# Kernel optimization log

Hardware: AMD Instinct MI355X
Metric: run time of the kernel (lower is better)

Reference implementation:

```python
import jax, jax.numpy as jnp
import numpy as np


def setup_inputs() -> dict:
    key = jax.random.key(0)
    ks = jax.random.split(key, 6)
    B, d, S = 256, 512, 196  # batch, hidden dim, spatial locations (14x14)
    return {
        "memory_state": jax.random.normal(ks[0], (B, d), dtype=jnp.float32),
        "ctrl_state": jax.random.normal(ks[1], (B, d), dtype=jnp.float32),
        "kb_proj": jax.random.normal(ks[2], (B, d, S), dtype=jnp.float32),
        "W_concat": jax.random.normal(ks[3], (d, d), dtype=jnp.float32) * (1.0 / np.sqrt(d)),
        "b_concat": jax.random.normal(ks[4], (d,), dtype=jnp.float32) * 0.01,
        "w_attn": jax.random.normal(ks[5], (d,), dtype=jnp.float32) * (1.0 / np.sqrt(d)),
    }


def reference(memory_state, ctrl_state, kb_proj, W_concat, b_concat, w_attn):
    # I_elements: [B, S, d] -- elementwise gating of knowledge base by memory
    I_t = memory_state[:, :, None] * kb_proj           # [B, d, S]
    I_t = jnp.transpose(I_t, (0, 2, 1))                # [B, S, d]
    # concat_layer (torch Linear: x @ W^T + b) + residual with kb_proj
    concat = jnp.einsum('bsd,ed->bse', I_t, W_concat) + b_concat
    concat = concat + jnp.transpose(kb_proj, (0, 2, 1))  # [B, S, d]
    # attention logits: (concat * ctrl) @ w_attn -> [B, S]
    rai = jnp.einsum('bsd,d->bs', concat * ctrl_state[:, None, :], w_attn)
    rvi = jax.nn.softmax(rai, axis=1)                  # [B, S]
    # attention-weighted sum over spatial locations -> [B, d]
    read_vector = jnp.einsum('bs,bds->bd', rvi, kb_proj)
    return read_vector
```

## Files before the change

### kernel.cpp

```cpp
#include <hip/hip_runtime.h>
#include <math.h>

#define B 256
#define D 512
#define S 196
#define SQ 49
#define NCH 8

__global__ __launch_bounds__(256, 8) void k_fused_logits(
    const float* __restrict__ kb, const float* __restrict__ mem,
    const float* __restrict__ ctrl, const float* __restrict__ w_attn,
    const float* __restrict__ W, float* __restrict__ rai_part) {
    __shared__ float u_s[D];
    __shared__ float gred[16][64];
    __shared__ float p_s[64];
    __shared__ float part[4][S];
    const int bid = blockIdx.x;
    const int b = bid >> 3, c = bid & 7;
    const int t = threadIdx.x;
    const int w = t >> 6, l = t & 63;

    u_s[t]       = ctrl[(size_t)b * D + t]       * w_attn[t];
    u_s[t + 256] = ctrl[(size_t)b * D + t + 256] * w_attn[t + 256];
    __syncthreads();

    {
        const int q = t & 15, eg = t >> 4;
        float4 g4 = {0.f, 0.f, 0.f, 0.f};
        const float* wbase = W + (size_t)c * 64 + 4 * q;
#pragma unroll 4
        for (int k = 0; k < 32; ++k) {
            const int e = k * 16 + eg;
            const float4 w4 = *(const float4*)(wbase + (size_t)e * D);
            const float uv = u_s[e];
            g4.x += uv * w4.x; g4.y += uv * w4.y;
            g4.z += uv * w4.z; g4.w += uv * w4.w;
        }
        *(float4*)&gred[eg][4 * q] = g4;
    }
    __syncthreads();
    if (t < 64) {
        float g = 0.f;
#pragma unroll
        for (int eg = 0; eg < 16; ++eg) g += gred[eg][t];
        const int d = c * 64 + t;
        p_s[t] = mem[(size_t)b * D + d] * g + u_s[d];
    }
    __syncthreads();

    const float* base = kb + (size_t)b * D * S + (size_t)c * 64 * S;
    if (l < SQ) {
        float4 acc0 = {0.f, 0.f, 0.f, 0.f}, acc1 = {0.f, 0.f, 0.f, 0.f};
        for (int i = 0; i < 8; ++i) {
            const int r0 = w * 16 + i, r1 = w * 16 + 8 + i;
            const float4 v0 = *(const float4*)(base + (size_t)r0 * S + 4 * l);
            const float4 v1 = *(const float4*)(base + (size_t)r1 * S + 4 * l);
            const float pv0 = p_s[r0], pv1 = p_s[r1];
            acc0.x += pv0 * v0.x; acc0.y += pv0 * v0.y;
            acc0.z += pv0 * v0.z; acc0.w += pv0 * v0.w;
            acc1.x += pv1 * v1.x; acc1.y += pv1 * v1.y;
            acc1.z += pv1 * v1.z; acc1.w += pv1 * v1.w;
        }
        part[w][4 * l + 0] = acc0.x + acc1.x;
        part[w][4 * l + 1] = acc0.y + acc1.y;
        part[w][4 * l + 2] = acc0.z + acc1.z;
        part[w][4 * l + 3] = acc0.w + acc1.w;
    }
    __syncthreads();
    if (t < S)
        rai_part[(size_t)bid * S + t] =
            (part[0][t] + part[1][t]) + (part[2][t] + part[3][t]);
}

__global__ __launch_bounds__(256, 8) void k_wsum(
    const float* __restrict__ kb, const float* __restrict__ rai_part,
    float* __restrict__ out) {
    __shared__ float rvi_s[S];
    __shared__ float redm[4], reds[4];
    __shared__ float plds[64 * SQ];
    __shared__ float red2[4][64];
    const int bid = blockIdx.x;
    const int b = bid >> 3, c = bid & 7;
    const int t = threadIdx.x;
    const int w = t >> 6, l = t & 63;

    float rai = -INFINITY;
    if (t < S) {
        float v = 0.f;
#pragma unroll
        for (int k = 0; k < NCH; ++k)
            v += rai_part[((size_t)b * NCH + k) * S + t];
        rai = v;
    }
    float m = rai;
#pragma unroll
    for (int o = 1; o < 64; o <<= 1) m = fmaxf(m, __shfl_xor(m, o, 64));
    if (l == 0) redm[w] = m;
    __syncthreads();
    m = fmaxf(fmaxf(redm[0], redm[1]), fmaxf(redm[2], redm[3]));
    float ex = (t < S) ? __expf(rai - m) : 0.f;
    float sm = ex;
#pragma unroll
    for (int o = 1; o < 64; o <<= 1) sm += __shfl_xor(sm, o, 64);
    if (l == 0) reds[w] = sm;
    __syncthreads();
    const float li = (reds[0] + reds[1]) + (reds[2] + reds[3]);
    if (t < S) rvi_s[t] = ex / li;
    __syncthreads();

    float4 rv = {0.f, 0.f, 0.f, 0.f};
    if (l < SQ) rv = *(const float4*)&rvi_s[4 * l];
    const float* base = kb + (size_t)b * D * S + (size_t)c * 64 * S;
    if (l < SQ) {
#pragma unroll 2
        for (int i = 0; i < 8; ++i) {
            const int r0 = w * 16 + i, r1 = w * 16 + 8 + i;
            const float4 v0 = *(const float4*)(base + (size_t)r0 * S + 4 * l);
            const float4 v1 = *(const float4*)(base + (size_t)r1 * S + 4 * l);
            plds[r0 * SQ + l] =
                rv.x * v0.x + rv.y * v0.y + rv.z * v0.z + rv.w * v0.w;
            plds[r1 * SQ + l] =
                rv.x * v1.x + rv.y * v1.y + rv.z * v1.z + rv.w * v1.w;
        }
    }
    __syncthreads();
    {
        const int row = t & 63, seg = t >> 6;
        const int j0 = (seg * SQ) >> 2, j1 = ((seg + 1) * SQ) >> 2;
        float a = 0.f;
        for (int j = j0; j < j1; ++j) a += plds[row * SQ + j];
        red2[seg][row] = a;
    }
    __syncthreads();
    if (t < 64)
        out[(size_t)b * D + c * 64 + t] =
            (red2[0][t] + red2[1][t]) + (red2[2][t] + red2[3][t]);
}

extern "C" void kernel_launch(void* const* d_in, const int* in_sizes, int n_in,
                              void* d_out, int out_size, void* d_ws, size_t ws_size,
                              hipStream_t stream) {
    const float* mem  = (const float*)d_in[0];
    const float* ctrl = (const float*)d_in[1];
    const float* kb   = (const float*)d_in[2];
    const float* W    = (const float*)d_in[3];
    const float* wat  = (const float*)d_in[5];
    float* out = (float*)d_out;

    float* rai_part = (float*)d_ws;

    k_fused_logits<<<B * NCH, 256, 0, stream>>>(kb, mem, ctrl, wat, W, rai_part);
    k_wsum        <<<B * NCH, 256, 0, stream>>>(kb, rai_part, out);
}
```

Before: 192.0 us.

## Split W-projection into separate batched kernel reusing W across eight batches

```diff
diff --git a/kernel.cpp b/kernel.cpp
--- a/kernel.cpp
+++ b/kernel.cpp
@@ -7,47 +7,48 @@
 #define SQ 49
 #define NCH 8
 
-__global__ __launch_bounds__(256, 8) void k_fused_logits(
-    const float* __restrict__ kb, const float* __restrict__ mem,
-    const float* __restrict__ ctrl, const float* __restrict__ w_attn,
-    const float* __restrict__ W, float* __restrict__ rai_part) {
-    __shared__ float u_s[D];
-    __shared__ float gred[16][64];
+__global__ __launch_bounds__(256) void k_pvec(
+    const float* __restrict__ mem, const float* __restrict__ ctrl,
+    const float* __restrict__ w_attn, const float* __restrict__ W,
+    float* __restrict__ p) {
+    __shared__ float u_s[8][D];
+    const int c = blockIdx.x & 7;
+    const int b0 = (blockIdx.x >> 3) * 8;
+    const int t = threadIdx.x;
+#pragma unroll
+    for (int idx = t; idx < 8 * D; idx += 256) {
+        const int j = idx >> 9, e = idx & (D - 1);
+        u_s[j][e] = ctrl[(size_t)(b0 + j) * D + e] * w_attn[e];
+    }
+    __syncthreads();
+    const int d = t & 63;
+    const int j0 = (t >> 6) * 2, j1 = j0 + 1;
+    const float* wcol = W + (size_t)c * 64 + d;
+    float a0 = 0.f, a1 = 0.f;
+#pragma unroll 4
+    for (int e = 0; e < D; ++e) {
+        const float wv = wcol[(size_t)e * D];
+        a0 += u_s[j0][e] * wv;
+        a1 += u_s[j1][e] * wv;
+    }
+    const int dg = c * 64 + d;
+    p[(size_t)(b0 + j0) * D + dg] =
+        mem[(size_t)(b0 + j0) * D + dg] * a0 + u_s[j0][dg];
+    p[(size_t)(b0 + j1) * D + dg] =
+        mem[(size_t)(b0 + j1) * D + dg] * a1 + u_s[j1][dg];
+}
+
+__global__ __launch_bounds__(256, 8) void k_logits(
+    const float* __restrict__ kb, const float* __restrict__ p,
+    float* __restrict__ rai_part) {
     __shared__ float p_s[64];
     __shared__ float part[4][S];
     const int bid = blockIdx.x;
     const int b = bid >> 3, c = bid & 7;
     const int t = threadIdx.x;
     const int w = t >> 6, l = t & 63;
-
-    u_s[t]       = ctrl[(size_t)b * D + t]       * w_attn[t];
-    u_s[t + 256] = ctrl[(size_t)b * D + t + 256] * w_attn[t + 256];
+    if (t < 64) p_s[t] = p[(size_t)b * D + c * 64 + t];
     __syncthreads();
-
-    {
-        const int q = t & 15, eg = t >> 4;
-        float4 g4 = {0.f, 0.f, 0.f, 0.f};
-        const float* wbase = W + (size_t)c * 64 + 4 * q;
-#pragma unroll 4
-        for (int k = 0; k < 32; ++k) {
-            const int e = k * 16 + eg;
-            const float4 w4 = *(const float4*)(wbase + (size_t)e * D);
-            const float uv = u_s[e];
-            g4.x += uv * w4.x; g4.y += uv * w4.y;
-            g4.z += uv * w4.z; g4.w += uv * w4.w;
-        }
-        *(float4*)&gred[eg][4 * q] = g4;
-    }
-    __syncthreads();
-    if (t < 64) {
-        float g = 0.f;
-#pragma unroll
-        for (int eg = 0; eg < 16; ++eg) g += gred[eg][t];
-        const int d = c * 64 + t;
-        p_s[t] = mem[(size_t)b * D + d] * g + u_s[d];
-    }
-    __syncthreads();
-
     const float* base = kb + (size_t)b * D * S + (size_t)c * 64 * S;
     if (l < SQ) {
         float4 acc0 = {0.f, 0.f, 0.f, 0.f}, acc1 = {0.f, 0.f, 0.f, 0.f};
@@ -147,8 +148,10 @@
     const float* wat  = (const float*)d_in[5];
     float* out = (float*)d_out;
 
-    float* rai_part = (float*)d_ws;
+    float* p        = (float*)d_ws;
+    float* rai_part = p + (size_t)B * D;
 
-    k_fused_logits<<<B * NCH, 256, 0, stream>>>(kb, mem, ctrl, wat, W, rai_part);
-    k_wsum        <<<B * NCH, 256, 0, stream>>>(kb, rai_part, out);
+    k_pvec  <<<256,     256, 0, stream>>>(mem, ctrl, wat, W, p);
+    k_logits<<<B * NCH, 256, 0, stream>>>(kb, p, rai_part);
+    k_wsum  <<<B * NCH, 256, 0, stream>>>(kb, rai_part, out);
 }
```

Result: slower. 244.7 us (+27.5%).

## Split u·W GEMM into batched kernel and fuse logits, softmax, weighted sum per batch

Applied to the files above, without the earlier changes.

```diff
diff --git a/kernel.cpp b/kernel.cpp
--- a/kernel.cpp
+++ b/kernel.cpp
@@ -7,52 +7,73 @@
 #define SQ 49
 #define NCH 8
 
-__global__ __launch_bounds__(256, 8) void k_fused_logits(
-    const float* __restrict__ kb, const float* __restrict__ mem,
+__global__ __launch_bounds__(256) void k_gemm2(
     const float* __restrict__ ctrl, const float* __restrict__ w_attn,
-    const float* __restrict__ W, float* __restrict__ rai_part) {
-    __shared__ float u_s[D];
-    __shared__ float gred[16][64];
-    __shared__ float p_s[64];
-    __shared__ float part[4][S];
-    const int bid = blockIdx.x;
-    const int b = bid >> 3, c = bid & 7;
+    const float* __restrict__ W, float* __restrict__ gpart) {
+    __shared__ float u_s[64][8];
+    const int ce = blockIdx.x >> 6;
+    const int dh = (blockIdx.x >> 5) & 1;
+    const int b0 = (blockIdx.x & 31) * 8;
+    const int t = threadIdx.x;
+    const int d = dh * 256 + t;
+#pragma unroll
+    for (int k = t; k < 512; k += 256) {
+        const int j = k & 7, el = k >> 3;
+        const int e = ce * 64 + el;
+        u_s[el][j] = ctrl[(size_t)(b0 + j) * D + e] * w_attn[e];
+    }
+    __syncthreads();
+    float a[8];
+#pragma unroll
+    for (int j = 0; j < 8; ++j) a[j] = 0.f;
+    for (int e0 = 0; e0 < 64; e0 += 4) {
+        float wv[4];
+#pragma unroll
+        for (int i = 0; i < 4; ++i)
+            wv[i] = W[(size_t)(ce * 64 + e0 + i) * D + d];
+#pragma unroll
+        for (int i = 0; i < 4; ++i) {
+            const float4 ua = *(const float4*)&u_s[e0 + i][0];
+            const float4 ub = *(const float4*)&u_s[e0 + i][4];
+            a[0] += ua.x * wv[i]; a[1] += ua.y * wv[i];
+            a[2] += ua.z * wv[i]; a[3] += ua.w * wv[i];
+            a[4] += ub.x * wv[i]; a[5] += ub.y * wv[i];
+            a[6] += ub.z * wv[i]; a[7] += ub.w * wv[i];
+        }
+    }
+#pragma unroll
+    for (int j = 0; j < 8; ++j)
+        gpart[((size_t)(b0 + j) * NCH + ce) * D + d] = a[j];
+}
+
+struct SmP2 { float plds[256 * SQ]; float red2[4][256]; };
+__global__ __launch_bounds__(1024, 1) void k_batch(
+    const float* __restrict__ kb, const float* __restrict__ gpart,
+    const float* __restrict__ mem, const float* __restrict__ ctrl,
+    const float* __restrict__ w_attn, float* __restrict__ out) {
+    __shared__ float p_s[D];
+    __shared__ float rvi_s[S];
+    __shared__ float redm[4], reds[4];
+    __shared__ union { float part[16][S]; SmP2 p2; } smu;
+    const int b = blockIdx.x;
     const int t = threadIdx.x;
     const int w = t >> 6, l = t & 63;
+    const float* base = kb + (size_t)b * D * S;
 
-    u_s[t]       = ctrl[(size_t)b * D + t]       * w_attn[t];
-    u_s[t + 256] = ctrl[(size_t)b * D + t + 256] * w_attn[t + 256];
-    __syncthreads();
-
-    {
-        const int q = t & 15, eg = t >> 4;
-        float4 g4 = {0.f, 0.f, 0.f, 0.f};
-        const float* wbase = W + (size_t)c * 64 + 4 * q;
-#pragma unroll 4
-        for (int k = 0; k < 32; ++k) {
-            const int e = k * 16 + eg;
-            const float4 w4 = *(const float4*)(wbase + (size_t)e * D);
-            const float uv = u_s[e];
-            g4.x += uv * w4.x; g4.y += uv * w4.y;
-            g4.z += uv * w4.z; g4.w += uv * w4.w;
-        }
-        *(float4*)&gred[eg][4 * q] = g4;
-    }
-    __syncthreads();
-    if (t < 64) {
-        float g = 0.f;
+    if (t < D) {
+        float s = 0.f;
 #pragma unroll
-        for (int eg = 0; eg < 16; ++eg) g += gred[eg][t];
-        const int d = c * 64 + t;
-        p_s[t] = mem[(size_t)b * D + d] * g + u_s[d];
+        for (int ce = 0; ce < NCH; ++ce)
+            s += gpart[((size_t)b * NCH + ce) * D + t];
+        p_s[t] = mem[(size_t)b * D + t] * s +
+                 ctrl[(size_t)b * D + t] * w_attn[t];
     }
     __syncthreads();
 
-    const float* base = kb + (size_t)b * D * S + (size_t)c * 64 * S;
     if (l < SQ) {
         float4 acc0 = {0.f, 0.f, 0.f, 0.f}, acc1 = {0.f, 0.f, 0.f, 0.f};
-        for (int i = 0; i < 8; ++i) {
-            const int r0 = w * 16 + i, r1 = w * 16 + 8 + i;
+        for (int i = 0; i < 16; ++i) {
+            const int r0 = w * 32 + i, r1 = w * 32 + 16 + i;
             const float4 v0 = *(const float4*)(base + (size_t)r0 * S + 4 * l);
             const float4 v1 = *(const float4*)(base + (size_t)r1 * S + 4 * l);
             const float pv0 = p_s[r0], pv1 = p_s[r1];
@@ -61,80 +82,75 @@
             acc1.x += pv1 * v1.x; acc1.y += pv1 * v1.y;
             acc1.z += pv1 * v1.z; acc1.w += pv1 * v1.w;
         }
-        part[w][4 * l + 0] = acc0.x + acc1.x;
-        part[w][4 * l + 1] = acc0.y + acc1.y;
-        part[w][4 * l + 2] = acc0.z + acc1.z;
-        part[w][4 * l + 3] = acc0.w + acc1.w;
+        smu.part[w][4 * l + 0] = acc0.x + acc1.x;
+        smu.part[w][4 * l + 1] = acc0.y + acc1.y;
+        smu.part[w][4 * l + 2] = acc0.z + acc1.z;
+        smu.part[w][4 * l + 3] = acc0.w + acc1.w;
     }
     __syncthreads();
-    if (t < S)
-        rai_part[(size_t)bid * S + t] =
-            (part[0][t] + part[1][t]) + (part[2][t] + part[3][t]);
-}
 
-__global__ __launch_bounds__(256, 8) void k_wsum(
-    const float* __restrict__ kb, const float* __restrict__ rai_part,
-    float* __restrict__ out) {
-    __shared__ float rvi_s[S];
-    __shared__ float redm[4], reds[4];
-    __shared__ float plds[64 * SQ];
-    __shared__ float red2[4][64];
-    const int bid = blockIdx.x;
-    const int b = bid >> 3, c = bid & 7;
-    const int t = threadIdx.x;
-    const int w = t >> 6, l = t & 63;
-
-    float rai = -INFINITY;
+    float rai = -INFINITY, ex = 0.f;
     if (t < S) {
         float v = 0.f;
 #pragma unroll
-        for (int k = 0; k < NCH; ++k)
-            v += rai_part[((size_t)b * NCH + k) * S + t];
+        for (int ww = 0; ww < 16; ++ww) v += smu.part[ww][t];
         rai = v;
     }
-    float m = rai;
+    if (t < 256) {
+        float m = rai;
 #pragma unroll
-    for (int o = 1; o < 64; o <<= 1) m = fmaxf(m, __shfl_xor(m, o, 64));
-    if (l == 0) redm[w] = m;
+        for (int o = 1; o < 64; o <<= 1) m = fmaxf(m, __shfl_xor(m, o, 64));
+        if (l == 0) redm[w] = m;
+    }
     __syncthreads();
-    m = fmaxf(fmaxf(redm[0], redm[1]), fmaxf(redm[2], redm[3]));
-    float ex = (t < S) ? __expf(rai - m) : 0.f;
-    float sm = ex;
+    if (t < 256) {
+        const float m = fmaxf(fmaxf(redm[0], redm[1]), fmaxf(redm[2], redm[3]));
+        ex = (t < S) ? __expf(rai - m) : 0.f;
+        float sm = ex;
 #pragma unroll
-    for (int o = 1; o < 64; o <<= 1) sm += __shfl_xor(sm, o, 64);
-    if (l == 0) reds[w] = sm;
+        for (int o = 1; o < 64; o <<= 1) sm += __shfl_xor(sm, o, 64);
+        if (l == 0) reds[w] = sm;
+    }
     __syncthreads();
-    const float li = (reds[0] + reds[1]) + (reds[2] + reds[3]);
-    if (t < S) rvi_s[t] = ex / li;
+    if (t < S) {
+        const float li = (reds[0] + reds[1]) + (reds[2] + reds[3]);
+        rvi_s[t] = ex / li;
+    }
     __syncthreads();
 
     float4 rv = {0.f, 0.f, 0.f, 0.f};
     if (l < SQ) rv = *(const float4*)&rvi_s[4 * l];
-    const float* base = kb + (size_t)b * D * S + (size_t)c * 64 * S;
-    if (l < SQ) {
+    for (int half = 0; half < 2; ++half) {
+        const int rb = half * 256;
+        if (l < SQ) {
 #pragma unroll 2
-        for (int i = 0; i < 8; ++i) {
-            const int r0 = w * 16 + i, r1 = w * 16 + 8 + i;
-            const float4 v0 = *(const float4*)(base + (size_t)r0 * S + 4 * l);
-            const float4 v1 = *(const float4*)(base + (size_t)r1 * S + 4 * l);
-            plds[r0 * SQ + l] =
-                rv.x * v0.x + rv.y * v0.y + rv.z * v0.z + rv.w * v0.w;
-            plds[r1 * SQ + l] =
-                rv.x * v1.x + rv.y * v1.y + rv.z * v1.z + rv.w * v1.w;
+            for (int i = 0; i < 8; ++i) {
+                const int q0 = w * 16 + i, q1 = w * 16 + 8 + i;
+                const float4 v0 =
+                    *(const float4*)(base + (size_t)(rb + q0) * S + 4 * l);
+                const float4 v1 =
+                    *(const float4*)(base + (size_t)(rb + q1) * S + 4 * l);
+                smu.p2.plds[q0 * SQ + l] =
+                    rv.x * v0.x + rv.y * v0.y + rv.z * v0.z + rv.w * v0.w;
+                smu.p2.plds[q1 * SQ + l] =
+                    rv.x * v1.x + rv.y * v1.y + rv.z * v1.z + rv.w * v1.w;
+            }
         }
+        __syncthreads();
+        {
+            const int r = t & 255, seg = t >> 8;
+            const int j0 = (seg * SQ) >> 2, j1 = ((seg + 1) * SQ) >> 2;
+            float a = 0.f;
+            for (int j = j0; j < j1; ++j) a += smu.p2.plds[r * SQ + j];
+            smu.p2.red2[seg][r] = a;
+        }
+        __syncthreads();
+        if (t < 256)
+            out[(size_t)b * D + rb + t] =
+                (smu.p2.red2[0][t] + smu.p2.red2[1][t]) +
+                (smu.p2.red2[2][t] + smu.p2.red2[3][t]);
+        __syncthreads();
     }
-    __syncthreads();
-    {
-        const int row = t & 63, seg = t >> 6;
-        const int j0 = (seg * SQ) >> 2, j1 = ((seg + 1) * SQ) >> 2;
-        float a = 0.f;
-        for (int j = j0; j < j1; ++j) a += plds[row * SQ + j];
-        red2[seg][row] = a;
-    }
-    __syncthreads();
-    if (t < 64)
-        out[(size_t)b * D + c * 64 + t] =
-            (red2[0][t] + red2[1][t]) + (red2[2][t] + red2[3][t]);
 }
 
 extern "C" void kernel_launch(void* const* d_in, const int* in_sizes, int n_in,
@@ -147,8 +163,8 @@
     const float* wat  = (const float*)d_in[5];
     float* out = (float*)d_out;
 
-    float* rai_part = (float*)d_ws;
+    float* gpart = (float*)d_ws;
 
-    k_fused_logits<<<B * NCH, 256, 0, stream>>>(kb, mem, ctrl, wat, W, rai_part);
-    k_wsum        <<<B * NCH, 256, 0, stream>>>(kb, rai_part, out);
+    k_gemm2<<<512, 256,  0, stream>>>(ctrl, wat, W, gpart);
+    k_batch<<<B,   1024, 0, stream>>>(kb, gpart, mem, ctrl, wat, out);
 }
```

Result: faster. 182.5 us (-4.9%).

## Split W·u matvec into batched GEMM kernel and prefetch kb rows early

Applied to the files above, without the earlier changes.

```diff
diff --git a/kernel.cpp b/kernel.cpp
--- a/kernel.cpp
+++ b/kernel.cpp
@@ -7,64 +7,108 @@
 #define SQ 49
 #define NCH 8
 
-__global__ __launch_bounds__(256, 8) void k_fused_logits(
-    const float* __restrict__ kb, const float* __restrict__ mem,
+__global__ __launch_bounds__(256) void k_gemm2(
     const float* __restrict__ ctrl, const float* __restrict__ w_attn,
-    const float* __restrict__ W, float* __restrict__ rai_part) {
-    __shared__ float u_s[D];
-    __shared__ float gred[16][64];
+    const float* __restrict__ W, float* __restrict__ gpart) {
+    __shared__ float u_s[64][8];
+    const int ce = blockIdx.x >> 6;
+    const int dh = (blockIdx.x >> 5) & 1;
+    const int b0 = (blockIdx.x & 31) * 8;
+    const int t = threadIdx.x;
+    const int d = dh * 256 + t;
+#pragma unroll
+    for (int k = t; k < 512; k += 256) {
+        const int j = k & 7, el = k >> 3;
+        const int e = ce * 64 + el;
+        u_s[el][j] = ctrl[(size_t)(b0 + j) * D + e] * w_attn[e];
+    }
+    __syncthreads();
+    float a[8];
+#pragma unroll
+    for (int j = 0; j < 8; ++j) a[j] = 0.f;
+    for (int e0 = 0; e0 < 64; e0 += 4) {
+        float wv[4];
+#pragma unroll
+        for (int i = 0; i < 4; ++i)
+            wv[i] = W[(size_t)(ce * 64 + e0 + i) * D + d];
+#pragma unroll
+        for (int i = 0; i < 4; ++i) {
+            const float4 ua = *(const float4*)&u_s[e0 + i][0];
+            const float4 ub = *(const float4*)&u_s[e0 + i][4];
+            a[0] += ua.x * wv[i]; a[1] += ua.y * wv[i];
+            a[2] += ua.z * wv[i]; a[3] += ua.w * wv[i];
+            a[4] += ub.x * wv[i]; a[5] += ub.y * wv[i];
+            a[6] += ub.z * wv[i]; a[7] += ub.w * wv[i];
+        }
+    }
+#pragma unroll
+    for (int j = 0; j < 8; ++j)
+        gpart[((size_t)(b0 + j) * NCH + ce) * D + d] = a[j];
+}
+
+__global__ __launch_bounds__(256, 4) void k_logits(
+    const float* __restrict__ kb, const float* __restrict__ gpart,
+    const float* __restrict__ mem, const float* __restrict__ ctrl,
+    const float* __restrict__ w_attn, float* __restrict__ rai_part) {
+    __shared__ float ph[4][64];
     __shared__ float p_s[64];
     __shared__ float part[4][S];
     const int bid = blockIdx.x;
     const int b = bid >> 3, c = bid & 7;
     const int t = threadIdx.x;
     const int w = t >> 6, l = t & 63;
-
-    u_s[t]       = ctrl[(size_t)b * D + t]       * w_attn[t];
-    u_s[t + 256] = ctrl[(size_t)b * D + t + 256] * w_attn[t + 256];
-    __syncthreads();
-
+    const float* base = kb + (size_t)b * D * S + (size_t)c * 64 * S;
+    const int r0 = w * 16;
+
+    float4 h0, h1, h2, h3;
+    if (l < SQ) {
+        h0 = *(const float4*)(base + (size_t)(r0 + 0) * S + 4 * l);
+        h1 = *(const float4*)(base + (size_t)(r0 + 1) * S + 4 * l);
+        h2 = *(const float4*)(base + (size_t)(r0 + 2) * S + 4 * l);
+        h3 = *(const float4*)(base + (size_t)(r0 + 3) * S + 4 * l);
+    }
     {
-        const int q = t & 15, eg = t >> 4;
-        float4 g4 = {0.f, 0.f, 0.f, 0.f};
-        const float* wbase = W + (size_t)c * 64 + 4 * q;
-#pragma unroll 4
-        for (int k = 0; k < 32; ++k) {
-            const int e = k * 16 + eg;
-            const float4 w4 = *(const float4*)(wbase + (size_t)e * D);
-            const float uv = u_s[e];
-            g4.x += uv * w4.x; g4.y += uv * w4.y;
-            g4.z += uv * w4.z; g4.w += uv * w4.w;
-        }
-        *(float4*)&gred[eg][4 * q] = g4;
+        const int d = c * 64 + l;
+        ph[w][l] = gpart[((size_t)b * NCH + w) * D + d] +
+                   gpart[((size_t)b * NCH + w + 4) * D + d];
     }
     __syncthreads();
     if (t < 64) {
-        float g = 0.f;
-#pragma unroll
-        for (int eg = 0; eg < 16; ++eg) g += gred[eg][t];
         const int d = c * 64 + t;
-        p_s[t] = mem[(size_t)b * D + d] * g + u_s[d];
-    }
-    __syncthreads();
-
-    const float* base = kb + (size_t)b * D * S + (size_t)c * 64 * S;
-    if (l < SQ) {
-        float4 acc0 = {0.f, 0.f, 0.f, 0.f}, acc1 = {0.f, 0.f, 0.f, 0.f};
-        for (int i = 0; i < 8; ++i) {
-            const int r0 = w * 16 + i, r1 = w * 16 + 8 + i;
-            const float4 v0 = *(const float4*)(base + (size_t)r0 * S + 4 * l);
-            const float4 v1 = *(const float4*)(base + (size_t)r1 * S + 4 * l);
-            const float pv0 = p_s[r0], pv1 = p_s[r1];
-            acc0.x += pv0 * v0.x; acc0.y += pv0 * v0.y;
-            acc0.z += pv0 * v0.z; acc0.w += pv0 * v0.w;
-            acc1.x += pv1 * v1.x; acc1.y += pv1 * v1.y;
-            acc1.z += pv1 * v1.z; acc1.w += pv1 * v1.w;
-        }
-        part[w][4 * l + 0] = acc0.x + acc1.x;
-        part[w][4 * l + 1] = acc0.y + acc1.y;
-        part[w][4 * l + 2] = acc0.z + acc1.z;
-        part[w][4 * l + 3] = acc0.w + acc1.w;
+        const float g = (ph[0][t] + ph[1][t]) + (ph[2][t] + ph[3][t]);
+        p_s[t] = mem[(size_t)b * D + d] * g +
+                 ctrl[(size_t)b * D + d] * w_attn[d];
+    }
+    __syncthreads();
+
+    if (l < SQ) {
+        float4 a0, a1, a2, a3;
+        {
+            const float p0 = p_s[r0 + 0], p1 = p_s[r0 + 1];
+            const float p2 = p_s[r0 + 2], p3 = p_s[r0 + 3];
+            a0.x = p0 * h0.x; a0.y = p0 * h0.y; a0.z = p0 * h0.z; a0.w = p0 * h0.w;
+            a1.x = p1 * h1.x; a1.y = p1 * h1.y; a1.z = p1 * h1.z; a1.w = p1 * h1.w;
+            a2.x = p2 * h2.x; a2.y = p2 * h2.y; a2.z = p2 * h2.z; a2.w = p2 * h2.w;
+            a3.x = p3 * h3.x; a3.y = p3 * h3.y; a3.z = p3 * h3.z; a3.w = p3 * h3.w;
+        }
+#pragma unroll
+        for (int i = 1; i < 4; ++i) {
+            const int r = r0 + 4 * i;
+            const float4 v0 = *(const float4*)(base + (size_t)(r + 0) * S + 4 * l);
+            const float4 v1 = *(const float4*)(base + (size_t)(r + 1) * S + 4 * l);
+            const float4 v2 = *(const float4*)(base + (size_t)(r + 2) * S + 4 * l);
+            const float4 v3 = *(const float4*)(base + (size_t)(r + 3) * S + 4 * l);
+            const float p0 = p_s[r + 0], p1 = p_s[r + 1];
+            const float p2 = p_s[r + 2], p3 = p_s[r + 3];
+            a0.x += p0 * v0.x; a0.y += p0 * v0.y; a0.z += p0 * v0.z; a0.w += p0 * v0.w;
+            a1.x += p1 * v1.x; a1.y += p1 * v1.y; a1.z += p1 * v1.z; a1.w += p1 * v1.w;
+            a2.x += p2 * v2.x; a2.y += p2 * v2.y; a2.z += p2 * v2.z; a2.w += p2 * v2.w;
+            a3.x += p3 * v3.x; a3.y += p3 * v3.y; a3.z += p3 * v3.z; a3.w += p3 * v3.w;
+        }
+        part[w][4 * l + 0] = (a0.x + a1.x) + (a2.x + a3.x);
+        part[w][4 * l + 1] = (a0.y + a1.y) + (a2.y + a3.y);
+        part[w][4 * l + 2] = (a0.z + a1.z) + (a2.z + a3.z);
+        part[w][4 * l + 3] = (a0.w + a1.w) + (a2.w + a3.w);
     }
     __syncthreads();
     if (t < S)
@@ -72,7 +116,7 @@
             (part[0][t] + part[1][t]) + (part[2][t] + part[3][t]);
 }
 
-__global__ __launch_bounds__(256, 8) void k_wsum(
+__global__ __launch_bounds__(256, 4) void k_wsum(
     const float* __restrict__ kb, const float* __restrict__ rai_part,
     float* __restrict__ out) {
     __shared__ float rvi_s[S];
@@ -83,7 +127,16 @@
     const int b = bid >> 3, c = bid & 7;
     const int t = threadIdx.x;
     const int w = t >> 6, l = t & 63;
-
+    const float* base = kb + (size_t)b * D * S + (size_t)c * 64 * S;
+    const int r0 = w * 16;
+
+    float4 h0, h1, h2, h3;
+    if (l < SQ) {
+        h0 = *(const float4*)(base + (size_t)(r0 + 0) * S + 4 * l);
+        h1 = *(const float4*)(base + (size_t)(r0 + 1) * S + 4 * l);
+        h2 = *(const float4*)(base + (size_t)(r0 + 2) * S + 4 * l);
+        h3 = *(const float4*)(base + (size_t)(r0 + 3) * S + 4 * l);
+    }
     float rai = -INFINITY;
     if (t < S) {
         float v = 0.f;
@@ -109,18 +162,31 @@
     __syncthreads();
 
     float4 rv = {0.f, 0.f, 0.f, 0.f};
-    if (l < SQ) rv = *(const float4*)&rvi_s[4 * l];
-    const float* base = kb + (size_t)b * D * S + (size_t)c * 64 * S;
-    if (l < SQ) {
-#pragma unroll 2
-        for (int i = 0; i < 8; ++i) {
-            const int r0 = w * 16 + i, r1 = w * 16 + 8 + i;
-            const float4 v0 = *(const float4*)(base + (size_t)r0 * S + 4 * l);
-            const float4 v1 = *(const float4*)(base + (size_t)r1 * S + 4 * l);
-            plds[r0 * SQ + l] =
+    if (l < SQ) {
+        rv = *(const float4*)&rvi_s[4 * l];
+        plds[(r0 + 0) * SQ + l] =
+            rv.x * h0.x + rv.y * h0.y + rv.z * h0.z + rv.w * h0.w;
+        plds[(r0 + 1) * SQ + l] =
+            rv.x * h1.x + rv.y * h1.y + rv.z * h1.z + rv.w * h1.w;
+        plds[(r0 + 2) * SQ + l] =
+            rv.x * h2.x + rv.y * h2.y + rv.z * h2.z + rv.w * h2.w;
+        plds[(r0 + 3) * SQ + l] =
+            rv.x * h3.x + rv.y * h3.y + rv.z * h3.z + rv.w * h3.w;
+#pragma unroll
+        for (int i = 1; i < 4; ++i) {
+            const int r = r0 + 4 * i;
+            const float4 v0 = *(const float4*)(base + (size_t)(r + 0) * S + 4 * l);
+            const float4 v1 = *(const float4*)(base + (size_t)(r + 1) * S + 4 * l);
+            const float4 v2 = *(const float4*)(base + (size_t)(r + 2) * S + 4 * l);
+            const float4 v3 = *(const float4*)(base + (size_t)(r + 3) * S + 4 * l);
+            plds[(r + 0) * SQ + l] =
                 rv.x * v0.x + rv.y * v0.y + rv.z * v0.z + rv.w * v0.w;
-            plds[r1 * SQ + l] =
+            plds[(r + 1) * SQ + l] =
                 rv.x * v1.x + rv.y * v1.y + rv.z * v1.z + rv.w * v1.w;
+            plds[(r + 2) * SQ + l] =
+                rv.x * v2.x + rv.y * v2.y + rv.z * v2.z + rv.w * v2.w;
+            plds[(r + 3) * SQ + l] =
+                rv.x * v3.x + rv.y * v3.y + rv.z * v3.z + rv.w * v3.w;
         }
     }
     __syncthreads();
@@ -147,8 +213,10 @@
     const float* wat  = (const float*)d_in[5];
     float* out = (float*)d_out;
 
-    float* rai_part = (float*)d_ws;
-
-    k_fused_logits<<<B * NCH, 256, 0, stream>>>(kb, mem, ctrl, wat, W, rai_part);
-    k_wsum        <<<B * NCH, 256, 0, stream>>>(kb, rai_part, out);
-}
+    float* gpart    = (float*)d_ws;
+    float* rai_part = gpart + (size_t)B * NCH * D;
+
+    k_gemm2 <<<512,     256, 0, stream>>>(ctrl, wat, W, gpart);
+    k_logits<<<B * NCH, 256, 0, stream>>>(kb, gpart, mem, ctrl, wat, rai_part);
+    k_wsum  <<<B * NCH, 256, 0, stream>>>(kb, rai_part, out);
+}
```

After: 187.4 us. 2.4% less time.
